# Kernel optimization log

Measured on AMD Instinct MI355X. Metric: run time of the kernel, lower is better.

## Reference

```python
import jax, jax.numpy as jnp
import numpy as np

B, IN, OUT, GD, TD, H, W, L = 16, 512, 256, 256, 256, 32, 32, 32
EPS_BN = 1e-5


def _conv2d(x, w, pad):
    return jax.lax.conv_general_dilated(
        x, w, window_strides=(1, 1), padding=[(pad, pad), (pad, pad)],
        dimension_numbers=("NCHW", "OIHW", "NCHW"))


def _up2(x):
    return jnp.repeat(jnp.repeat(x, 2, axis=2), 2, axis=3)


def _l2n(v):  # F.normalize(p=2, dim=1), eps=1e-12
    n = jnp.sqrt(jnp.sum(v * v, axis=1, keepdims=True))
    return v / jnp.maximum(n, 1e-12)


def _context(img_embs, words_embs, mask):
    i = _l2n(img_embs)            # [B, TD, P]
    wd = _l2n(words_embs)         # [B, TD, L]
    sim = jnp.einsum("bcp,bcl->bpl", i, wd)
    sim = jnp.where(mask[:, None, :], -jnp.inf, sim)
    attn = jax.nn.softmax(sim, axis=-1)
    return jnp.einsum("bpl,bcl->bcp", attn, wd)  # [B, TD, P]


def _bn(x, w, b):  # training-mode BatchNorm2d, biased variance
    m = jnp.mean(x, axis=(0, 2, 3), keepdims=True)
    v = jnp.var(x, axis=(0, 2, 3), keepdims=True)
    return (x - m) * jax.lax.rsqrt(v + EPS_BN) * w[None, :, None, None] + b[None, :, None, None]


def setup_inputs():
    key = jax.random.key(0)
    ks = jax.random.split(key, 16)
    s = 0.02
    COND = GD + TD
    return {
        "x": jax.random.normal(ks[0], (B, IN, H, W), jnp.float32),
        "global_cond": jax.random.normal(ks[1], (B, GD), jnp.float32),
        "words_embs": jax.random.normal(ks[2], (B, TD, L), jnp.float32),
        "mask": jax.random.randint(ks[3], (B, L), 0, 2).astype(bool),
        "w_img1": jax.random.normal(ks[4], (TD, IN), jnp.float32) * s,
        "w_img2": jax.random.normal(ks[5], (TD, OUT), jnp.float32) * s,
        "w_c1": jax.random.normal(ks[6], (OUT, IN, 3, 3), jnp.float32) * s,
        "w_c2": jax.random.normal(ks[7], (OUT, OUT, 3, 3), jnp.float32) * s,
        "bn1_w": jnp.ones((IN,), jnp.float32),
        "bn1_b": jnp.zeros((IN,), jnp.float32),
        "bn2_w": jnp.ones((OUT,), jnp.float32),
        "bn2_b": jnp.zeros((OUT,), jnp.float32),
        "w_g1": jax.random.normal(ks[8], (IN, COND), jnp.float32) * s,
        "b_g1": jnp.zeros((IN,), jnp.float32),
        "w_b1": jax.random.normal(ks[9], (IN, COND), jnp.float32) * s,
        "b_b1": jnp.zeros((IN,), jnp.float32),
        "w_g2": jax.random.normal(ks[10], (OUT, COND), jnp.float32) * s,
        "b_g2": jnp.zeros((OUT,), jnp.float32),
        "w_b2": jax.random.normal(ks[11], (OUT, COND), jnp.float32) * s,
        "b_b2": jnp.zeros((OUT,), jnp.float32),
        "w_sc": jax.random.normal(ks[12], (OUT, IN, 1, 1), jnp.float32) * s,
        "b_sc": jnp.zeros((OUT,), jnp.float32),
    }


def reference(x, global_cond, words_embs, mask,
              w_img1, w_img2, w_c1, w_c2,
              bn1_w, bn1_b, bn2_w, bn2_b,
              w_g1, b_g1, w_b1, b_b1,
              w_g2, b_g2, w_b2, b_b2,
              w_sc, b_sc):
    # ---- residual path, stage 1 ----
    img1 = jnp.einsum("tc,bcp->btp", w_img1, x.reshape(B, IN, H * W))
    ctx1 = _context(img1, words_embs, mask)                 # [B, TD, H*W]
    gc = jnp.broadcast_to(global_cond[:, :, None], (B, GD, H * W))
    cond1 = jnp.concatenate([gc, ctx1], axis=1)             # [B, GD+TD, H*W]
    gamma1 = jnp.einsum("oc,bcp->bop", w_g1, cond1) + b_g1[None, :, None]
    beta1 = jnp.einsum("oc,bcp->bop", w_b1, cond1) + b_b1[None, :, None]
    out = gamma1.reshape(B, IN, H, W) * _bn(x, bn1_w, bn1_b) + beta1.reshape(B, IN, H, W)
    out = jax.nn.relu(out)
    out = _up2(out)                                         # [B, IN, 2H, 2W]
    out = _conv2d(out, w_c1, 1)                             # [B, OUT, 2H, 2W]
    h2, w2 = 2 * H, 2 * W
    # ---- residual path, stage 2 ----
    img2 = jnp.einsum("tc,bcp->btp", w_img2, out.reshape(B, OUT, h2 * w2))
    ctx2 = _context(img2, words_embs, mask)                 # [B, TD, h2*w2]
    gc2 = jnp.broadcast_to(global_cond[:, :, None], (B, GD, h2 * w2))
    cond2 = jnp.concatenate([gc2, ctx2], axis=1)
    gamma2 = jnp.einsum("oc,bcp->bop", w_g2, cond2) + b_g2[None, :, None]
    beta2 = jnp.einsum("oc,bcp->bop", w_b2, cond2) + b_b2[None, :, None]
    out = gamma2.reshape(B, OUT, h2, w2) * _bn(out, bn2_w, bn2_b) + beta2.reshape(B, OUT, h2, w2)
    out = jax.nn.relu(out)
    out = _conv2d(out, w_c2, 1)
    # ---- shortcut ----
    sc = _conv2d(_up2(x), w_sc, 0) + b_sc[None, :, None, None]
    return out + sc
```

## Files before the change

### kernel.cpp

```cpp
#include <hip/hip_runtime.h>
#include <hip/hip_bf16.h>
#include <math.h>

#define NB 16
#define CIN1 512
#define COUT 256
#define GD 256
#define TD 256
#define LL 32
#define P1 1024
#define P2 4096
#define CONDC 512

typedef __attribute__((ext_vector_type(8))) short bf16x8;
typedef __attribute__((ext_vector_type(4))) float f32x4;
typedef unsigned short u16;

__device__ __forceinline__ u16 f2b(float f) {
  __hip_bfloat16 h = __float2bfloat16(f);
  return *(u16*)&h;
}
__device__ __forceinline__ float b2f(u16 v) {
  unsigned u = ((unsigned)v) << 16;
  float f;
  __builtin_memcpy(&f, &u, 4);
  return f;
}

__global__ void bn_stats_x_kernel(const float* __restrict__ x, float* __restrict__ mean,
                                  float* __restrict__ rstd, u16* __restrict__ xbf,
                                  int C, int HW) {
  int c = blockIdx.x, t = threadIdx.x;
  float s = 0.f, sq = 0.f;
  for (int b = 0; b < NB; ++b) {
    size_t base = ((size_t)b * C + c) * HW;
    for (int i = t; i < HW; i += 256) {
      float v = x[base + i];
      s += v; sq += v * v;
      xbf[base + i] = f2b(v);
    }
  }
  __shared__ float ss[256], sq2[256];
  ss[t] = s; sq2[t] = sq; __syncthreads();
  for (int o = 128; o > 0; o >>= 1) {
    if (t < o) { ss[t] += ss[t + o]; sq2[t] += sq2[t + o]; }
    __syncthreads();
  }
  if (t == 0) {
    float n = (float)NB * (float)HW;
    float m = ss[0] / n;
    float v = sq2[0] / n - m * m;
    mean[c] = m;
    rstd[c] = rsqrtf(v + 1e-5f);
  }
}

__global__ void bn_fin_kernel(const float* __restrict__ part, float* __restrict__ mean,
                              float* __restrict__ rstd) {
  int c = threadIdx.x;
  float s = 0.f, sq = 0.f;
  const float* ps = part + (size_t)c * 256;
  const float* pq = part + 65536 + (size_t)c * 256;
  for (int i = 0; i < 256; ++i) { s += ps[i]; sq += pq[i]; }
  float n = 16.f * 4096.f;
  float m = s / n;
  mean[c] = m;
  rstd[c] = rsqrtf(sq / n - m * m + 1e-5f);
}

__global__ void wdn_kernel(const float* __restrict__ we, float* __restrict__ wdn) {
  int b = blockIdx.x >> 5, l = blockIdx.x & 31;
  int t = threadIdx.x;
  const float* base = we + (size_t)b * TD * LL + l;
  float v[4]; float sq = 0.f;
#pragma unroll
  for (int k = 0; k < 4; ++k) { v[k] = base[(size_t)(t * 4 + k) * LL]; sq += v[k] * v[k]; }
#pragma unroll
  for (int o = 32; o > 0; o >>= 1) sq += __shfl_xor(sq, o);
  float r = 1.f / fmaxf(sqrtf(sq), 1e-12f);
  float* ob = wdn + (size_t)b * TD * LL + l;
#pragma unroll
  for (int k = 0; k < 4; ++k) ob[(size_t)(t * 4 + k) * LL] = v[k] * r;
}

__global__ __launch_bounds__(256) void attnctx_kernel(
    const u16* __restrict__ img, const float* __restrict__ wdn,
    const int* __restrict__ mask, u16* __restrict__ ctx, int P) {
  __shared__ u16 imgT[2][64 * 72];
  __shared__ u16 wdnT[32 * 264];
  __shared__ u16 wdnC[256 * 40];
  __shared__ u16 attnB[64 * 40];
  __shared__ float sqP[4][64];
  __shared__ float rnL[64];
  const int b = blockIdx.y, p0 = blockIdx.x * 64;
  const int tid = threadIdx.x;
  const int w = tid >> 6, lane = tid & 63;
  const int l15 = lane & 15, lg = lane >> 4;
  const u16* ib = img + (size_t)b * TD * P;
  const float* wb = wdn + (size_t)b * TD * LL;

  for (int i = tid; i < TD * LL; i += 256) {
    int t = i >> 5, l = i & 31;
    u16 v = f2b(wb[i]);
    wdnT[l * 264 + t] = v;
    wdnC[t * 40 + l] = v;
  }

  f32x4 s0 = {}, s1 = {};
  float ssq = 0.f;
  unsigned pk[8];
#pragma unroll
  for (int i = 0; i < 8; ++i) {
    int t = w * 16 + 2 * i;
    u16 h0 = ib[(size_t)t * P + p0 + lane];
    u16 h1 = ib[(size_t)(t + 1) * P + p0 + lane];
    float v0 = b2f(h0), v1 = b2f(h1);
    ssq += v0 * v0 + v1 * v1;
    pk[i] = (unsigned)h0 | ((unsigned)h1 << 16);
  }
#pragma unroll
  for (int i = 0; i < 8; ++i)
    *(unsigned*)(imgT[0] + lane * 72 + w * 16 + 2 * i) = pk[i];
  __syncthreads();

  for (int q = 0; q < 4; ++q) {
    const int cur = q & 1;
    if (q < 3) {
#pragma unroll
      for (int i = 0; i < 8; ++i) {
        int t = (q + 1) * 64 + w * 16 + 2 * i;
        u16 h0 = ib[(size_t)t * P + p0 + lane];
        u16 h1 = ib[(size_t)(t + 1) * P + p0 + lane];
        float v0 = b2f(h0), v1 = b2f(h1);
        ssq += v0 * v0 + v1 * v1;
        pk[i] = (unsigned)h0 | ((unsigned)h1 << 16);
      }
    }
#pragma unroll
    for (int ks = 0; ks < 2; ++ks) {
      bf16x8 a = *(const bf16x8*)(imgT[cur] + (w * 16 + l15) * 72 + ks * 32 + lg * 8);
      bf16x8 b0 = *(const bf16x8*)(wdnT + l15 * 264 + q * 64 + ks * 32 + lg * 8);
      bf16x8 b1 = *(const bf16x8*)(wdnT + (16 + l15) * 264 + q * 64 + ks * 32 + lg * 8);
      s0 = __builtin_amdgcn_mfma_f32_16x16x32_bf16(a, b0, s0, 0, 0, 0);
      s1 = __builtin_amdgcn_mfma_f32_16x16x32_bf16(a, b1, s1, 0, 0, 0);
    }
    if (q < 3) {
#pragma unroll
      for (int i = 0; i < 8; ++i)
        *(unsigned*)(imgT[cur ^ 1] + lane * 72 + w * 16 + 2 * i) = pk[i];
      __syncthreads();
    }
  }
  sqP[w][lane] = ssq;
  __syncthreads();
  if (tid < 64) {
    float s = sqP[0][tid] + sqP[1][tid] + sqP[2][tid] + sqP[3][tid];
    rnL[tid] = 1.f / fmaxf(sqrtf(s), 1e-12f);
  }
  __syncthreads();
  const bool m0 = mask[b * LL + l15] != 0;
  const bool m1 = mask[b * LL + 16 + l15] != 0;
#pragma unroll
  for (int k = 0; k < 4; ++k) {
    float rn = rnL[w * 16 + lg * 4 + k];
    float v0 = m0 ? -INFINITY : s0[k] * rn;
    float v1 = m1 ? -INFINITY : s1[k] * rn;
    float mx = fmaxf(v0, v1);
#pragma unroll
    for (int o = 1; o < 16; o <<= 1) mx = fmaxf(mx, __shfl_xor(mx, o));
    float e0 = expf(v0 - mx), e1 = expf(v1 - mx);
    float sm = e0 + e1;
#pragma unroll
    for (int o = 1; o < 16; o <<= 1) sm += __shfl_xor(sm, o);
    float inv = 1.f / sm;
    int px = w * 16 + lg * 4 + k;
    attnB[px * 40 + l15] = f2b(e0 * inv);
    attnB[px * 40 + 16 + l15] = f2b(e1 * inv);
  }
  __syncthreads();
  f32x4 acc[4][4] = {};
  bf16x8 bfr[4];
#pragma unroll
  for (int pt = 0; pt < 4; ++pt)
    bfr[pt] = *(const bf16x8*)(attnB + (pt * 16 + l15) * 40 + lg * 8);
#pragma unroll
  for (int cc = 0; cc < 4; ++cc) {
    bf16x8 a = *(const bf16x8*)(wdnC + ((w * 4 + cc) * 16 + l15) * 40 + lg * 8);
#pragma unroll
    for (int pt = 0; pt < 4; ++pt)
      acc[cc][pt] = __builtin_amdgcn_mfma_f32_16x16x32_bf16(a, bfr[pt], acc[cc][pt], 0, 0, 0);
  }
#pragma unroll
  for (int cc = 0; cc < 4; ++cc) {
#pragma unroll
    for (int pt = 0; pt < 4; ++pt) {
#pragma unroll
      for (int k = 0; k < 4; ++k) {
        int c = (w * 4 + cc) * 16 + lg * 4 + k;
        ctx[((size_t)b * TD + c) * P + p0 + pt * 16 + l15] = f2b(acc[cc][pt][k]);
      }
    }
  }
}

template <bool XB, bool YB>
__global__ __launch_bounds__(256, 2) void gemm_mfma_kernel(
    const float* __restrict__ W, int ldw, int c_off,
    const void* __restrict__ Xv, const float* __restrict__ vec,
    void* __restrict__ Yv, int T, int C, int P) {
  __shared__ u16 Wl[2][128 * 44];
  __shared__ u16 Xl[2][128 * 40];
  const int b = blockIdx.z;
  const int t0 = blockIdx.y * 128, p0 = blockIdx.x * 128;
  const int tid = threadIdx.x;
  const int w = tid >> 6, lane = tid & 63;
  const int wo = w >> 1, wq = w & 1;
  const int l15 = lane & 15, lg = lane >> 4;
  const int wr = tid >> 1, wcH = tid & 1;
  const int xr = tid >> 3, xcG = tid & 7;
  const int csw = xr ^ ((xcG & 3) << 3);
  const float* wsrc = W + (size_t)(t0 + wr) * ldw + c_off + wcH * 16;
  const float* xsrc32 = XB ? nullptr : (const float*)Xv + (size_t)b * C * P + (size_t)xr * P + p0 + xcG * 16;
  const u16* xsrc16 = XB ? (const u16*)Xv + (size_t)b * C * P + (size_t)xr * P + p0 + xcG * 16 : nullptr;
  const int NK = C / 32;
  f32x4 acc[4][4] = {};
  float4 wreg[4];
  u16 xst[16];

#pragma unroll
  for (int j = 0; j < 4; ++j) wreg[j] = *(const float4*)(wsrc + j * 4);
  if (XB) {
    union { u16 u[16]; uint4 q[2]; } xu;
    xu.q[0] = *(const uint4*)(xsrc16);
    xu.q[1] = *(const uint4*)(xsrc16 + 8);
#pragma unroll
    for (int i = 0; i < 16; ++i) xst[i] = xu.u[i];
  } else {
#pragma unroll
    for (int j = 0; j < 4; ++j) {
      float4 v = *(const float4*)(xsrc32 + j * 4);
      xst[j * 4 + 0] = f2b(v.x); xst[j * 4 + 1] = f2b(v.y);
      xst[j * 4 + 2] = f2b(v.z); xst[j * 4 + 3] = f2b(v.w);
    }
  }
  {
    u16* dst = Wl[0] + wr * 44 + wcH * 16;
#pragma unroll
    for (int j = 0; j < 4; ++j)
      *(ushort4*)(dst + j * 4) = make_ushort4(f2b(wreg[j].x), f2b(wreg[j].y), f2b(wreg[j].z), f2b(wreg[j].w));
#pragma unroll
    for (int i = 0; i < 16; ++i)
      Xl[0][(xcG * 16 + i) * 40 + csw] = xst[i];
  }
  __syncthreads();

  for (int kb = 0; kb < NK; ++kb) {
    const int cur = kb & 1;
    if (kb + 1 < NK) {
      const int c0n = (kb + 1) * 32;
#pragma unroll
      for (int j = 0; j < 4; ++j) wreg[j] = *(const float4*)(wsrc + c0n + j * 4);
      if (XB) {
        union { u16 u[16]; uint4 q[2]; } xu;
        xu.q[0] = *(const uint4*)(xsrc16 + (size_t)c0n * P);
        xu.q[1] = *(const uint4*)(xsrc16 + (size_t)c0n * P + 8);
#pragma unroll
        for (int i = 0; i < 16; ++i) xst[i] = xu.u[i];
      } else {
#pragma unroll
        for (int j = 0; j < 4; ++j) {
          float4 v = *(const float4*)(xsrc32 + (size_t)c0n * P + j * 4);
          xst[j * 4 + 0] = f2b(v.x); xst[j * 4 + 1] = f2b(v.y);
          xst[j * 4 + 2] = f2b(v.z); xst[j * 4 + 3] = f2b(v.w);
        }
      }
    }
    bf16x8 a[4], bb[4];
#pragma unroll
    for (int rr = 0; rr < 4; ++rr)
      a[rr] = *(const bf16x8*)(Wl[cur] + (wo * 64 + rr * 16 + l15) * 44 + lg * 8);
#pragma unroll
    for (int ss = 0; ss < 4; ++ss)
      bb[ss] = *(const bf16x8*)(Xl[cur] + (wq * 64 + ss * 16 + l15) * 40 + ((lg ^ ss) << 3));
#pragma unroll
    for (int rr = 0; rr < 4; ++rr)
#pragma unroll
      for (int ss = 0; ss < 4; ++ss)
        acc[rr][ss] = __builtin_amdgcn_mfma_f32_16x16x32_bf16(a[rr], bb[ss], acc[rr][ss], 0, 0, 0);
    if (kb + 1 < NK) {
      const int nxt = cur ^ 1;
      u16* dst = Wl[nxt] + wr * 44 + wcH * 16;
#pragma unroll
      for (int j = 0; j < 4; ++j)
        *(ushort4*)(dst + j * 4) = make_ushort4(f2b(wreg[j].x), f2b(wreg[j].y), f2b(wreg[j].z), f2b(wreg[j].w));
#pragma unroll
      for (int i = 0; i < 16; ++i)
        Xl[nxt][(xcG * 16 + i) * 40 + csw] = xst[i];
      __syncthreads();
    }
  }
#pragma unroll
  for (int rr = 0; rr < 4; ++rr) {
    int tb = t0 + wo * 64 + rr * 16 + lg * 4;
#pragma unroll
    for (int ss = 0; ss < 4; ++ss) {
      int p = p0 + wq * 64 + ss * 16 + l15;
#pragma unroll
      for (int k = 0; k < 4; ++k) {
        int t = tb + k;
        float val = acc[rr][ss][k];
        if (vec) val += vec[(size_t)b * T + t];
        if (YB) ((u16*)Yv)[((size_t)b * T + t) * P + p] = f2b(val);
        else    ((float*)Yv)[((size_t)b * T + t) * P + p] = val;
      }
    }
  }
}

template <bool XINB>
__global__ __launch_bounds__(256, 2) void gbact_kernel(
    const float* __restrict__ Wg, const float* __restrict__ bg,
    const float* __restrict__ Wb, const float* __restrict__ bb_,
    const u16* __restrict__ ctx, const float* __restrict__ gcond,
    const void* __restrict__ xinv,
    const float* __restrict__ mean, const float* __restrict__ rstd,
    const float* __restrict__ bnw, const float* __restrict__ bnb,
    u16* __restrict__ outb, int C, int P) {
  __shared__ u16 shmem[2][16384];
  __shared__ float gvl[128], bvl[128];
  const int b = blockIdx.z, t0 = blockIdx.y * 128, p0 = blockIdx.x * 128;
  const int tid = threadIdx.x;
  const int w = tid >> 6, lane = tid & 63;
  const int wo = w >> 1, wq = w & 1;
  const int l15 = lane & 15, lg = lane >> 4;
  const int wr = tid >> 1, wcH = tid & 1;
  const int xr = tid >> 3, xcG = tid & 7;
  const int csw = xr ^ ((xcG & 3) << 3);
  const float* gsrc = Wg + (size_t)(t0 + wr) * CONDC + GD + wcH * 16;
  const float* bsrc = Wb + (size_t)(t0 + wr) * CONDC + GD + wcH * 16;
  const u16* xsrc = ctx + (size_t)b * TD * P + (size_t)xr * P + p0 + xcG * 16;
  const int NK = TD / 32;
  f32x4 accg[4][4] = {}, accb[4][4] = {};
  float4 greg[4], breg[4];
  u16 xst[16];

  {
    int t = tid & 127;
    const float* row = (tid < 128 ? Wg : Wb) + (size_t)(t0 + t) * CONDC;
    const float* gc = gcond + (size_t)b * GD;
    float s = 0.f;
    for (int c = 0; c < GD; c += 4) {
      float4 wv = *(const float4*)(row + c);
      float4 gv4 = *(const float4*)(gc + c);
      s += wv.x * gv4.x + wv.y * gv4.y + wv.z * gv4.z + wv.w * gv4.w;
    }
    s += (tid < 128 ? bg : bb_)[t0 + t];
    if (tid < 128) gvl[t] = s; else bvl[t] = s;
  }

#pragma unroll
  for (int j = 0; j < 4; ++j) {
    greg[j] = *(const float4*)(gsrc + j * 4);
    breg[j] = *(const float4*)(bsrc + j * 4);
  }
  {
    union { u16 u[16]; uint4 q[2]; } xu;
    xu.q[0] = *(const uint4*)(xsrc);
    xu.q[1] = *(const uint4*)(xsrc + 8);
#pragma unroll
    for (int i = 0; i < 16; ++i) xst[i] = xu.u[i];
  }
  {
    u16* dg = shmem[0] + wr * 44 + wcH * 16;
    u16* db = shmem[0] + 5632 + wr * 44 + wcH * 16;
    u16* xl = shmem[0] + 11264;
#pragma unroll
    for (int j = 0; j < 4; ++j) {
      *(ushort4*)(dg + j * 4) = make_ushort4(f2b(greg[j].x), f2b(greg[j].y), f2b(greg[j].z), f2b(greg[j].w));
      *(ushort4*)(db + j * 4) = make_ushort4(f2b(breg[j].x), f2b(breg[j].y), f2b(breg[j].z), f2b(breg[j].w));
    }
#pragma unroll
    for (int i = 0; i < 16; ++i)
      xl[(xcG * 16 + i) * 40 + csw] = xst[i];
  }
  __syncthreads();

  for (int kb = 0; kb < NK; ++kb) {
    const int cur = kb & 1;
    if (kb + 1 < NK) {
      const int c0n = (kb + 1) * 32;
#pragma unroll
      for (int j = 0; j < 4; ++j) {
        greg[j] = *(const float4*)(gsrc + c0n + j * 4);
        breg[j] = *(const float4*)(bsrc + c0n + j * 4);
      }
      union { u16 u[16]; uint4 q[2]; } xu;
      xu.q[0] = *(const uint4*)(xsrc + (size_t)c0n * P);
      xu.q[1] = *(const uint4*)(xsrc + (size_t)c0n * P + 8);
#pragma unroll
      for (int i = 0; i < 16; ++i) xst[i] = xu.u[i];
    }
    bf16x8 ag[4], ab[4], bb[4];
#pragma unroll
    for (int rr = 0; rr < 4; ++rr) {
      ag[rr] = *(const bf16x8*)(shmem[cur] + (wo * 64 + rr * 16 + l15) * 44 + lg * 8);
      ab[rr] = *(const bf16x8*)(shmem[cur] + 5632 + (wo * 64 + rr * 16 + l15) * 44 + lg * 8);
    }
#pragma unroll
    for (int ss = 0; ss < 4; ++ss)
      bb[ss] = *(const bf16x8*)(shmem[cur] + 11264 + (wq * 64 + ss * 16 + l15) * 40 + ((lg ^ ss) << 3));
#pragma unroll
    for (int rr = 0; rr < 4; ++rr)
#pragma unroll
      for (int ss = 0; ss < 4; ++ss) {
        accg[rr][ss] = __builtin_amdgcn_mfma_f32_16x16x32_bf16(ag[rr], bb[ss], accg[rr][ss], 0, 0, 0);
        accb[rr][ss] = __builtin_amdgcn_mfma_f32_16x16x32_bf16(ab[rr], bb[ss], accb[rr][ss], 0, 0, 0);
      }
    if (kb + 1 < NK) {
      const int nxt = cur ^ 1;
      u16* dg = shmem[nxt] + wr * 44 + wcH * 16;
      u16* db = shmem[nxt] + 5632 + wr * 44 + wcH * 16;
      u16* xl = shmem[nxt] + 11264;
#pragma unroll
      for (int j = 0; j < 4; ++j) {
        *(ushort4*)(dg + j * 4) = make_ushort4(f2b(greg[j].x), f2b(greg[j].y), f2b(greg[j].z), f2b(greg[j].w));
        *(ushort4*)(db + j * 4) = make_ushort4(f2b(breg[j].x), f2b(breg[j].y), f2b(breg[j].z), f2b(breg[j].w));
      }
#pragma unroll
      for (int i = 0; i < 16; ++i)
        xl[(xcG * 16 + i) * 40 + csw] = xst[i];
      __syncthreads();
    }
  }
  __syncthreads();
  u16* tbuf = &shmem[0][0];
#pragma unroll
  for (int rr = 0; rr < 4; ++rr) {
    float gv[4], bv[4], mm[4], rs[4], bB[4];
#pragma unroll
    for (int k = 0; k < 4; ++k) {
      int cl = wo * 64 + rr * 16 + lg * 4 + k;
      int c = t0 + cl;
      gv[k] = gvl[cl];
      bv[k] = bvl[cl];
      mm[k] = mean[c]; rs[k] = rstd[c] * bnw[c]; bB[k] = bnb[c];
    }
#pragma unroll
    for (int ss = 0; ss < 4; ++ss) {
#pragma unroll
      for (int k = 0; k < 4; ++k) {
        int cl = wo * 64 + rr * 16 + lg * 4 + k;
        int pl = wq * 64 + ss * 16 + l15;
        size_t xidx = ((size_t)b * C + t0 + cl) * P + p0 + pl;
        float xv = XINB ? b2f(((const u16*)xinv)[xidx]) : ((const float*)xinv)[xidx];
        float g = accg[rr][ss][k] + gv[k];
        float be = accb[rr][ss][k] + bv[k];
        float val = fmaxf(g * ((xv - mm[k]) * rs[k] + bB[k]) + be, 0.f);
        tbuf[pl * 136 + cl] = f2b(val);
      }
    }
  }
  __syncthreads();
  const int pr = tid >> 1, h = tid & 1;
#pragma unroll
  for (int j = 0; j < 8; ++j) {
    uint4 v = *(uint4*)(tbuf + pr * 136 + h * 64 + j * 8);
    *(uint4*)(outb + ((size_t)b * P + p0 + pr) * C + t0 + h * 64 + j * 8) = v;
  }
}

__global__ void pack2_kernel(const float* __restrict__ w1, u16* __restrict__ wp1,
                             const float* __restrict__ w2, u16* __restrict__ wp2) {
  int lin = blockIdx.x * 256 + threadIdx.x;
  const int N1 = COUT * CIN1;
  const float* w; u16* wp; int CIN;
  if (lin < N1) { w = w1; wp = wp1; CIN = CIN1; }
  else { lin -= N1; if (lin >= COUT * COUT) return; w = w2; wp = wp2; CIN = COUT; }
  int o = lin / CIN, c = lin - o * CIN;
  int c0blk = c >> 5, lg = (c >> 3) & 3, cc = c & 7;
  int ot = o >> 4, l15 = o & 15;
  int lane = lg * 16 + l15;
  size_t base = (((size_t)c0blk * (COUT >> 4) + ot) * 64 + lane) * 8 + cc;
  size_t posStride = (size_t)(CIN >> 5) * (COUT >> 4) * 512;
  const float* src = w + ((size_t)o * CIN + c) * 9;
#pragma unroll
  for (int pos = 0; pos < 9; ++pos)
    wp[pos * posStride + base] = f2b(src[pos]);
}

template <int CIN, bool UP, bool OUTB, bool STATS>
__global__ __launch_bounds__(512, 2) void conv_mfma_kernel(
    const u16* __restrict__ Wp, const u16* __restrict__ Xt,
    const u16* __restrict__ scs, const float* __restrict__ scb,
    void* __restrict__ Yv, float* __restrict__ part) {
  constexpr int S = UP ? 32 : 64;
  constexpr int NC0 = CIN >> 5;
  constexpr int NCH = 6 * 66 * 8;
  __shared__ u16 Xs[2][6 * 66 * 36];
  __shared__ float stats_ls[256], stats_lsq[256];
  const int b = blockIdx.z, pxT = blockIdx.x;
  const int tid = threadIdx.x;
  const int w = tid >> 6, lane = tid & 63;
  const int wo = w >> 2, wp_ = w & 3;
  const int l15 = lane & 15, lg = lane >> 4;
  const int Y0 = pxT * 4;
  const u16* Xb = Xt + (size_t)b * S * S * CIN;
  const size_t posStride = (size_t)NC0 * 16 * 512;
  f32x4 acc[8][4] = {};
  uint2 st[7];

  if (STATS && tid < 256) { stats_ls[tid] = 0.f; stats_lsq[tid] = 0.f; }

#pragma unroll
  for (int j = 0; j < 7; ++j) {
    int i = tid + j * 512;
    if (i < NCH) {
      int r = i / 528, rem = i - r * 528, col = rem >> 3, ch = rem & 7;
      int uy = Y0 - 1 + r, ux = col - 1;
      uint2 v = make_uint2(0u, 0u);
      if (uy >= 0 && uy < 64 && ux >= 0 && ux < 64) {
        int sy = UP ? (uy >> 1) : uy, sx = UP ? (ux >> 1) : ux;
        v = *(const uint2*)(Xb + ((size_t)sy * S + sx) * CIN + ch * 4);
      }
      st[j] = v;
    }
  }
#pragma unroll
  for (int j = 0; j < 7; ++j) {
    int i = tid + j * 512;
    if (i < NCH) {
      int r = i / 528, rem = i - r * 528, col = rem >> 3, ch = rem & 7;
      *(uint2*)(&Xs[0][(r * 66 + col) * 36 + ch * 4]) = st[j];
    }
  }
  __syncthreads();

  for (int c0b = 0; c0b < NC0; ++c0b) {
    const int cur = c0b & 1;
    if (c0b + 1 < NC0) {
      const int c0n = (c0b + 1) << 5;
#pragma unroll
      for (int j = 0; j < 7; ++j) {
        int i = tid + j * 512;
        if (i < NCH) {
          int r = i / 528, rem = i - r * 528, col = rem >> 3, ch = rem & 7;
          int uy = Y0 - 1 + r, ux = col - 1;
          uint2 v = make_uint2(0u, 0u);
          if (uy >= 0 && uy < 64 && ux >= 0 && ux < 64) {
            int sy = UP ? (uy >> 1) : uy, sx = UP ? (ux >> 1) : ux;
            v = *(const uint2*)(Xb + ((size_t)sy * S + sx) * CIN + c0n + ch * 4);
          }
          st[j] = v;
        }
      }
    }
    {
      const u16* wbB = Wp + ((size_t)c0b * 16 + wo * 8) * 512 + lane * 8;
      bf16x8 aC[8], aN[8];
#pragma unroll
      for (int rr = 0; rr < 8; ++rr)
        aC[rr] = *(const bf16x8*)(wbB + rr * 512);
#pragma unroll
      for (int pos = 0; pos < 9; ++pos) {
        const int ky = pos / 3, kx = pos - ky * 3;
        if (pos < 8) {
          const u16* wbn = wbB + (size_t)(pos + 1) * posStride;
#pragma unroll
          for (int rr = 0; rr < 8; ++rr)
            aN[rr] = *(const bf16x8*)(wbn + rr * 512);
        }
        const int rowb = ((wp_ + ky) * 66 + kx) * 36 + lg * 8;
#pragma unroll
        for (int ss = 0; ss < 4; ++ss) {
          int idx = rowb + (ss * 16 + l15) * 36;
          union { uint2 q[2]; bf16x8 v; } u;
          u.q[0] = *(const uint2*)(&Xs[cur][idx]);
          u.q[1] = *(const uint2*)(&Xs[cur][idx + 4]);
#pragma unroll
          for (int rr = 0; rr < 8; ++rr)
            acc[rr][ss] = __builtin_amdgcn_mfma_f32_16x16x32_bf16(aC[rr], u.v, acc[rr][ss], 0, 0, 0);
        }
#pragma unroll
        for (int rr = 0; rr < 8; ++rr) aC[rr] = aN[rr];
      }
    }
    if (c0b + 1 < NC0) {
#pragma unroll
      for (int j = 0; j < 7; ++j) {
        int i = tid + j * 512;
        if (i < NCH) {
          int r = i / 528, rem = i - r * 528, col = rem >> 3, ch = rem & 7;
          *(uint2*)(&Xs[cur ^ 1][(r * 66 + col) * 36 + ch * 4]) = st[j];
        }
      }
      __syncthreads();
    }
  }
  const int oBase = wo * 128 + lg * 4;
  const int pxBase = pxT * 256 + wp_ * 64 + l15;
  const int y = Y0 + wp_;
#pragma unroll
  for (int rr = 0; rr < 8; ++rr) {
#pragma unroll
    for (int ss = 0; ss < 4; ++ss) {
      int px = pxBase + ss * 16;
#pragma unroll
      for (int k = 0; k < 4; ++k) {
        int o = oBase + rr * 16 + k;
        float val = acc[rr][ss][k];
        if (scs) {
          int gx = px & 63;
          val += b2f(scs[((size_t)b * COUT + o) * P1 + (y >> 1) * 32 + (gx >> 1)]) + scb[o];
        }
        if (OUTB) ((u16*)Yv)[((size_t)b * COUT + o) * 4096 + px] = f2b(val);
        else      ((float*)Yv)[((size_t)b * COUT + o) * 4096 + px] = val;
      }
    }
  }
  if (STATS) {
#pragma unroll
    for (int rr = 0; rr < 8; ++rr) {
#pragma unroll
      for (int k = 0; k < 4; ++k) {
        float s = acc[rr][0][k] + acc[rr][1][k] + acc[rr][2][k] + acc[rr][3][k];
        float sq = acc[rr][0][k] * acc[rr][0][k] + acc[rr][1][k] * acc[rr][1][k] +
                   acc[rr][2][k] * acc[rr][2][k] + acc[rr][3][k] * acc[rr][3][k];
#pragma unroll
        for (int o = 1; o < 16; o <<= 1) { s += __shfl_xor(s, o); sq += __shfl_xor(sq, o); }
        if (l15 == 0) {
          int o_ = oBase + rr * 16 + k;
          atomicAdd(&stats_ls[o_], s);
          atomicAdd(&stats_lsq[o_], sq);
        }
      }
    }
    __syncthreads();
    if (tid < 256) {
      int blk = b * 16 + pxT;
      part[(size_t)tid * 256 + blk] = stats_ls[tid];
      part[65536 + (size_t)tid * 256 + blk] = stats_lsq[tid];
    }
  }
}

extern "C" void kernel_launch(void* const* d_in, const int* in_sizes, int n_in,
                              void* d_out, int out_size, void* d_ws, size_t ws_size,
                              hipStream_t stream) {
  const float* x      = (const float*)d_in[0];
  const float* gcond  = (const float*)d_in[1];
  const float* wemb   = (const float*)d_in[2];
  const int*   mask   = (const int*)d_in[3];
  const float* w_img1 = (const float*)d_in[4];
  const float* w_img2 = (const float*)d_in[5];
  const float* w_c1   = (const float*)d_in[6];
  const float* w_c2   = (const float*)d_in[7];
  const float* bn1_w  = (const float*)d_in[8];
  const float* bn1_b  = (const float*)d_in[9];
  const float* bn2_w  = (const float*)d_in[10];
  const float* bn2_b  = (const float*)d_in[11];
  const float* w_g1   = (const float*)d_in[12];
  const float* b_g1   = (const float*)d_in[13];
  const float* w_b1   = (const float*)d_in[14];
  const float* b_b1   = (const float*)d_in[15];
  const float* w_g2   = (const float*)d_in[16];
  const float* b_g2   = (const float*)d_in[17];
  const float* w_b2   = (const float*)d_in[18];
  const float* b_b2   = (const float*)d_in[19];
  const float* w_sc   = (const float*)d_in[20];
  const float* b_sc   = (const float*)d_in[21];
  float* out = (float*)d_out;
  float* ws = (float*)d_ws;

  const size_t MF = 16777216;
  float* A  = ws;
  float* Br = ws + MF;
  float* Cr = ws + 2 * MF;
  float* SM = ws + 3 * MF;
  float* wdn   = SM;
  float* mean1 = SM + 131072;
  float* rstd1 = mean1 + 512;
  float* mean2 = rstd1 + 512;
  float* rstd2 = mean2 + 256;
  float* part  = rstd2 + 256;
  float* wsp   = part + 131072;
  u16* Wp1 = (u16*)wsp;
  u16* Wp2 = (u16*)(wsp + 655360);
  u16* scs = (u16*)(wsp + 655360 + 294912);

  u16* img1   = (u16*)A;
  u16* ctx1   = (u16*)A + 4194304;
  u16* Xt1    = (u16*)A + 8388608;
  u16* xbf    = (u16*)A + 16777216;
  u16* conv1o = (u16*)Cr;
  u16* img2   = (u16*)Br;
  u16* ctx2   = (u16*)A;
  u16* Xt2    = (u16*)Br;

  bn_stats_x_kernel<<<dim3(CIN1), dim3(256), 0, stream>>>(x, mean1, rstd1, xbf, CIN1, P1);
  wdn_kernel<<<dim3(NB * LL), dim3(64), 0, stream>>>(wemb, wdn);
  pack2_kernel<<<dim3((COUT * CIN1 + COUT * COUT) / 256), dim3(256), 0, stream>>>(
      w_c1, Wp1, w_c2, Wp2);
  gemm_mfma_kernel<true, true><<<dim3(P1 / 128, TD / 128, NB), dim3(256), 0, stream>>>(
      w_img1, CIN1, 0, xbf, nullptr, img1, TD, CIN1, P1);
  gemm_mfma_kernel<true, true><<<dim3(P1 / 128, COUT / 128, NB), dim3(256), 0, stream>>>(
      w_sc, CIN1, 0, xbf, nullptr, scs, COUT, CIN1, P1);
  attnctx_kernel<<<dim3(P1 / 64, NB), dim3(256), 0, stream>>>(img1, wdn, mask, ctx1, P1);
  gbact_kernel<true><<<dim3(P1 / 128, CIN1 / 128, NB), dim3(256), 0, stream>>>(
      w_g1, b_g1, w_b1, b_b1, ctx1, gcond, xbf, mean1, rstd1, bn1_w, bn1_b, Xt1, CIN1, P1);
  conv_mfma_kernel<CIN1, true, true, true><<<dim3(16, 1, NB), dim3(512), 0, stream>>>(
      Wp1, Xt1, nullptr, nullptr, conv1o, part);

  bn_fin_kernel<<<dim3(1), dim3(256), 0, stream>>>(part, mean2, rstd2);
  gemm_mfma_kernel<true, true><<<dim3(P2 / 128, TD / 128, NB), dim3(256), 0, stream>>>(
      w_img2, COUT, 0, conv1o, nullptr, img2, TD, COUT, P2);
  attnctx_kernel<<<dim3(P2 / 64, NB), dim3(256), 0, stream>>>(img2, wdn, mask, ctx2, P2);
  gbact_kernel<true><<<dim3(P2 / 128, COUT / 128, NB), dim3(256), 0, stream>>>(
      w_g2, b_g2, w_b2, b_b2, ctx2, gcond, conv1o, mean2, rstd2, bn2_w, bn2_b, Xt2, COUT, P2);
  conv_mfma_kernel<COUT, false, false, false><<<dim3(16, 1, NB), dim3(512), 0, stream>>>(
      Wp2, Xt2, scs, b_sc, out, nullptr);
}
```

Measured before the change: 461.3 us.

## Fuse stage-2 image projection GEMM into attention-context kernel

Stage 2 now computes the img2 projection (w_img2 times conv1 output) inside a new attnimg kernel. The img2 tensor stays in shared memory and is normalized in-register before the similarity, softmax and context MFMAs, so the separate GEMM launch and the img2 global round trip are gone. w_img2 is pre-packed into MFMA fragment layout by an extended pack kernel. The cost is that every 64-pixel block streams the full packed weight from global/L2 with no shared-memory reuse, and the blocks use more LDS and registers.

```diff
diff --git a/kernel.cpp b/kernel.cpp
--- a/kernel.cpp
+++ b/kernel.cpp
@@ -198,6 +198,153 @@
       for (int k = 0; k < 4; ++k) {
         int c = (w * 4 + cc) * 16 + lg * 4 + k;
         ctx[((size_t)b * TD + c) * P + p0 + pt * 16 + l15] = f2b(acc[cc][pt][k]);
+      }
+    }
+  }
+}
+
+__global__ __launch_bounds__(256) void attnimg_kernel(
+    const u16* __restrict__ W2p, const u16* __restrict__ xin,
+    const float* __restrict__ wdn, const int* __restrict__ mask,
+    u16* __restrict__ ctx, int P) {
+  __shared__ u16 smem[(33792 + 16896) / 2];
+  __shared__ float rnL[64];
+  u16* imgT  = smem;
+  u16* Xl    = smem + 16896;
+  u16* wdnT  = smem + 16896;
+  u16* wdnC  = smem;
+  u16* attnB = smem + 10240;
+  const int b = blockIdx.y, p0 = blockIdx.x * 64;
+  const int tid = threadIdx.x;
+  const int w = tid >> 6, lane = tid & 63;
+  const int l15 = lane & 15, lg = lane >> 4;
+  const u16* xb = xin + (size_t)b * COUT * P;
+  const float* wb = wdn + (size_t)b * TD * LL;
+
+  const int xr = tid >> 3, xcG = tid & 7;
+  const int csw = xr ^ (((xcG >> 1) & 3) << 3);
+  const u16* xsrc = xb + (size_t)xr * P + p0 + xcG * 8;
+  u16 xst[8];
+  {
+    union { u16 u[8]; uint4 q; } xu;
+    xu.q = *(const uint4*)xsrc;
+#pragma unroll
+    for (int i = 0; i < 8; ++i) xst[i] = xu.u[i];
+  }
+#pragma unroll
+  for (int i = 0; i < 8; ++i)
+    Xl[(xcG * 8 + i) * 40 + csw] = xst[i];
+  __syncthreads();
+
+  f32x4 acc[16];
+#pragma unroll
+  for (int tt = 0; tt < 16; ++tt) acc[tt] = (f32x4){0.f, 0.f, 0.f, 0.f};
+  for (int c0b = 0; c0b < 8; ++c0b) {
+    const int cur = c0b & 1;
+    if (c0b + 1 < 8) {
+      union { u16 u[8]; uint4 q; } xu;
+      xu.q = *(const uint4*)(xsrc + (size_t)((c0b + 1) * 32) * P);
+#pragma unroll
+      for (int i = 0; i < 8; ++i) xst[i] = xu.u[i];
+    }
+    bf16x8 aA = *(const bf16x8*)(Xl + cur * 2560 + (w * 16 + l15) * 40 + ((lg ^ w) << 3));
+#pragma unroll
+    for (int tt = 0; tt < 16; ++tt) {
+      bf16x8 bfr = *(const bf16x8*)(W2p + (((size_t)c0b * 16 + tt) * 64 + lane) * 8);
+      acc[tt] = __builtin_amdgcn_mfma_f32_16x16x32_bf16(aA, bfr, acc[tt], 0, 0, 0);
+    }
+    if (c0b + 1 < 8) {
+      const int nxt = cur ^ 1;
+#pragma unroll
+      for (int i = 0; i < 8; ++i)
+        Xl[nxt * 2560 + (xcG * 8 + i) * 40 + csw] = xst[i];
+      __syncthreads();
+    }
+  }
+#pragma unroll
+  for (int k = 0; k < 4; ++k) {
+    float s = 0.f;
+#pragma unroll
+    for (int tt = 0; tt < 16; ++tt) s += acc[tt][k] * acc[tt][k];
+#pragma unroll
+    for (int o = 1; o < 16; o <<= 1) s += __shfl_xor(s, o);
+    if (l15 == 0) rnL[w * 16 + lg * 4 + k] = 1.f / fmaxf(sqrtf(s), 1e-12f);
+  }
+#pragma unroll
+  for (int tt = 0; tt < 16; ++tt)
+#pragma unroll
+    for (int k = 0; k < 4; ++k)
+      imgT[(w * 16 + lg * 4 + k) * 264 + tt * 16 + l15] = f2b(acc[tt][k]);
+  __syncthreads();
+
+  for (int i = tid; i < TD * LL; i += 256) {
+    int t = i >> 5, l = i & 31;
+    wdnT[l * 264 + t] = f2b(wb[i]);
+  }
+  __syncthreads();
+  f32x4 s0 = {}, s1 = {};
+#pragma unroll
+  for (int q = 0; q < 4; ++q) {
+#pragma unroll
+    for (int ks = 0; ks < 2; ++ks) {
+      bf16x8 a = *(const bf16x8*)(imgT + (w * 16 + l15) * 264 + q * 64 + ks * 32 + lg * 8);
+      bf16x8 b0 = *(const bf16x8*)(wdnT + l15 * 264 + q * 64 + ks * 32 + lg * 8);
+      bf16x8 b1 = *(const bf16x8*)(wdnT + (16 + l15) * 264 + q * 64 + ks * 32 + lg * 8);
+      s0 = __builtin_amdgcn_mfma_f32_16x16x32_bf16(a, b0, s0, 0, 0, 0);
+      s1 = __builtin_amdgcn_mfma_f32_16x16x32_bf16(a, b1, s1, 0, 0, 0);
+    }
+  }
+  const bool m0 = mask[b * LL + l15] != 0;
+  const bool m1 = mask[b * LL + 16 + l15] != 0;
+  float a0[4], a1[4];
+#pragma unroll
+  for (int k = 0; k < 4; ++k) {
+    float rn = rnL[w * 16 + lg * 4 + k];
+    float v0 = m0 ? -INFINITY : s0[k] * rn;
+    float v1 = m1 ? -INFINITY : s1[k] * rn;
+    float mx = fmaxf(v0, v1);
+#pragma unroll
+    for (int o = 1; o < 16; o <<= 1) mx = fmaxf(mx, __shfl_xor(mx, o));
+    float e0 = expf(v0 - mx), e1 = expf(v1 - mx);
+    float sm = e0 + e1;
+#pragma unroll
+    for (int o = 1; o < 16; o <<= 1) sm += __shfl_xor(sm, o);
+    float inv = 1.f / sm;
+    a0[k] = e0 * inv; a1[k] = e1 * inv;
+  }
+  __syncthreads();
+
+  for (int i = tid; i < TD * LL; i += 256) {
+    int t = i >> 5, l = i & 31;
+    wdnC[t * 40 + l] = f2b(wb[i]);
+  }
+#pragma unroll
+  for (int k = 0; k < 4; ++k) {
+    int px = w * 16 + lg * 4 + k;
+    attnB[px * 40 + l15] = f2b(a0[k]);
+    attnB[px * 40 + 16 + l15] = f2b(a1[k]);
+  }
+  __syncthreads();
+  f32x4 acc2[4][4] = {};
+  bf16x8 bfr[4];
+#pragma unroll
+  for (int pt = 0; pt < 4; ++pt)
+    bfr[pt] = *(const bf16x8*)(attnB + (pt * 16 + l15) * 40 + lg * 8);
+#pragma unroll
+  for (int cc = 0; cc < 4; ++cc) {
+    bf16x8 a = *(const bf16x8*)(wdnC + ((w * 4 + cc) * 16 + l15) * 40 + lg * 8);
+#pragma unroll
+    for (int pt = 0; pt < 4; ++pt)
+      acc2[cc][pt] = __builtin_amdgcn_mfma_f32_16x16x32_bf16(a, bfr[pt], acc2[cc][pt], 0, 0, 0);
+  }
+#pragma unroll
+  for (int cc = 0; cc < 4; ++cc) {
+#pragma unroll
+    for (int pt = 0; pt < 4; ++pt) {
+#pragma unroll
+      for (int k = 0; k < 4; ++k) {
+        int c = (w * 4 + cc) * 16 + lg * 4 + k;
+        ctx[((size_t)b * TD + c) * P + p0 + pt * 16 + l15] = f2b(acc2[cc][pt][k]);
       }
     }
   }
@@ -469,23 +616,34 @@
   }
 }
 
-__global__ void pack2_kernel(const float* __restrict__ w1, u16* __restrict__ wp1,
-                             const float* __restrict__ w2, u16* __restrict__ wp2) {
+__global__ void pack3_kernel(const float* __restrict__ w1, u16* __restrict__ wp1,
+                             const float* __restrict__ w2, u16* __restrict__ wp2,
+                             const float* __restrict__ wi2, u16* __restrict__ w2p) {
   int lin = blockIdx.x * 256 + threadIdx.x;
   const int N1 = COUT * CIN1;
-  const float* w; u16* wp; int CIN;
-  if (lin < N1) { w = w1; wp = wp1; CIN = CIN1; }
-  else { lin -= N1; if (lin >= COUT * COUT) return; w = w2; wp = wp2; CIN = COUT; }
-  int o = lin / CIN, c = lin - o * CIN;
-  int c0blk = c >> 5, lg = (c >> 3) & 3, cc = c & 7;
-  int ot = o >> 4, l15 = o & 15;
-  int lane = lg * 16 + l15;
-  size_t base = (((size_t)c0blk * (COUT >> 4) + ot) * 64 + lane) * 8 + cc;
-  size_t posStride = (size_t)(CIN >> 5) * (COUT >> 4) * 512;
-  const float* src = w + ((size_t)o * CIN + c) * 9;
-#pragma unroll
-  for (int pos = 0; pos < 9; ++pos)
-    wp[pos * posStride + base] = f2b(src[pos]);
+  const int N2 = COUT * COUT;
+  if (lin < N1 + N2) {
+    const float* w; u16* wp; int CIN;
+    if (lin < N1) { w = w1; wp = wp1; CIN = CIN1; }
+    else { lin -= N1; w = w2; wp = wp2; CIN = COUT; }
+    int o = lin / CIN, c = lin - o * CIN;
+    int c0blk = c >> 5, lg = (c >> 3) & 3, cc = c & 7;
+    int ot = o >> 4, l15 = o & 15;
+    int lane = lg * 16 + l15;
+    size_t base = (((size_t)c0blk * (COUT >> 4) + ot) * 64 + lane) * 8 + cc;
+    size_t posStride = (size_t)(CIN >> 5) * (COUT >> 4) * 512;
+    const float* src = w + ((size_t)o * CIN + c) * 9;
+#pragma unroll
+    for (int pos = 0; pos < 9; ++pos)
+      wp[pos * posStride + base] = f2b(src[pos]);
+  } else {
+    lin -= N1 + N2;
+    if (lin >= COUT * COUT) return;
+    int t = lin >> 8, c = lin & 255;
+    int tt = t >> 4, l15 = t & 15;
+    int c0b = c >> 5, lg = (c >> 3) & 3, cc = c & 7;
+    w2p[(((size_t)c0b * 16 + tt) * 64 + lg * 16 + l15) * 8 + cc] = f2b(wi2[(size_t)t * COUT + c]);
+  }
 }
 
 template <int CIN, bool UP, bool OUTB, bool STATS>
@@ -686,20 +844,20 @@
   u16* Wp1 = (u16*)wsp;
   u16* Wp2 = (u16*)(wsp + 655360);
   u16* scs = (u16*)(wsp + 655360 + 294912);
+  u16* W2p = (u16*)(wsp + 655360 + 294912 + 2097152);
 
   u16* img1   = (u16*)A;
   u16* ctx1   = (u16*)A + 4194304;
   u16* Xt1    = (u16*)A + 8388608;
   u16* xbf    = (u16*)A + 16777216;
   u16* conv1o = (u16*)Cr;
-  u16* img2   = (u16*)Br;
   u16* ctx2   = (u16*)A;
   u16* Xt2    = (u16*)Br;
 
   bn_stats_x_kernel<<<dim3(CIN1), dim3(256), 0, stream>>>(x, mean1, rstd1, xbf, CIN1, P1);
   wdn_kernel<<<dim3(NB * LL), dim3(64), 0, stream>>>(wemb, wdn);
-  pack2_kernel<<<dim3((COUT * CIN1 + COUT * COUT) / 256), dim3(256), 0, stream>>>(
-      w_c1, Wp1, w_c2, Wp2);
+  pack3_kernel<<<dim3((COUT * CIN1 + 2 * COUT * COUT + 255) / 256), dim3(256), 0, stream>>>(
+      w_c1, Wp1, w_c2, Wp2, w_img2, W2p);
   gemm_mfma_kernel<true, true><<<dim3(P1 / 128, TD / 128, NB), dim3(256), 0, stream>>>(
       w_img1, CIN1, 0, xbf, nullptr, img1, TD, CIN1, P1);
   gemm_mfma_kernel<true, true><<<dim3(P1 / 128, COUT / 128, NB), dim3(256), 0, stream>>>(
@@ -711,9 +869,8 @@
       Wp1, Xt1, nullptr, nullptr, conv1o, part);
 
   bn_fin_kernel<<<dim3(1), dim3(256), 0, stream>>>(part, mean2, rstd2);
-  gemm_mfma_kernel<true, true><<<dim3(P2 / 128, TD / 128, NB), dim3(256), 0, stream>>>(
-      w_img2, COUT, 0, conv1o, nullptr, img2, TD, COUT, P2);
-  attnctx_kernel<<<dim3(P2 / 64, NB), dim3(256), 0, stream>>>(img2, wdn, mask, ctx2, P2);
+  attnimg_kernel<<<dim3(P2 / 64, NB), dim3(256), 0, stream>>>(
+      W2p, conv1o, wdn, mask, ctx2, P2);
   gbact_kernel<true><<<dim3(P2 / 128, COUT / 128, NB), dim3(256), 0, stream>>>(
       w_g2, b_g2, w_b2, b_b2, ctx2, gcond, conv1o, mean2, rstd2, bn2_w, bn2_b, Xt2, COUT, P2);
   conv_mfma_kernel<COUT, false, false, false><<<dim3(16, 1, NB), dim3(512), 0, stream>>>(
```

Result: no change. 458.1 us (-0.7%).
